# Kernel tuning notes

Measured on AMD Instinct MI355X. Metric: run time of the kernel, lower is better.

Reference implementation:

```python
import jax, jax.numpy as jnp
import numpy as np

B, T, IN, H = 262144, 15, 1, 64
BN_EPS = 1e-5


def _lstm_layer(xs, w_ih, w_hh, b):
    """xs: [T, B, in] -> (hs [T, B, H], h_last [B, H]). torch gate order i,f,g,o."""
    Bn = xs.shape[1]
    h0 = jnp.zeros((Bn, H), xs.dtype)
    c0 = jnp.zeros((Bn, H), xs.dtype)

    def step(carry, x_t):
        h, c = carry
        z = x_t @ w_ih.T + h @ w_hh.T + b  # [B, 4H]
        i, f, g, o = jnp.split(z, 4, axis=-1)
        i = jax.nn.sigmoid(i)
        f = jax.nn.sigmoid(f)
        g = jnp.tanh(g)
        o = jax.nn.sigmoid(o)
        c = f * c + i * g
        h = o * jnp.tanh(c)
        return (h, c), h

    (h_last, _), hs = jax.lax.scan(step, (h0, c0), xs)
    return hs, h_last


def setup_inputs() -> dict:
    key = jax.random.key(0)
    ks = jax.random.split(key, 12)
    s = 0.1  # weight init scale ~ 1/sqrt(H)
    return {
        "x": jax.random.normal(ks[0], (B, T, IN), jnp.float32),
        "bn_gamma": jnp.ones((T,), jnp.float32),
        "bn_beta": jnp.zeros((T,), jnp.float32),
        "w_ih0": jax.random.normal(ks[1], (4 * H, IN), jnp.float32) * s,
        "w_hh0": jax.random.normal(ks[2], (4 * H, H), jnp.float32) * s,
        "b_ih0": jax.random.normal(ks[3], (4 * H,), jnp.float32) * s,
        "b_hh0": jax.random.normal(ks[4], (4 * H,), jnp.float32) * s,
        "w_ih1": jax.random.normal(ks[5], (4 * H, H), jnp.float32) * s,
        "w_hh1": jax.random.normal(ks[6], (4 * H, H), jnp.float32) * s,
        "b_ih1": jax.random.normal(ks[7], (4 * H,), jnp.float32) * s,
        "b_hh1": jax.random.normal(ks[8], (4 * H,), jnp.float32) * s,
        "fc_w": jax.random.normal(ks[9], (H, H), jnp.float32) * s,
        "fc_b": jax.random.normal(ks[10], (H,), jnp.float32) * s,
    }


def reference(x, bn_gamma, bn_beta, w_ih0, w_hh0, b_ih0, b_hh0,
              w_ih1, w_hh1, b_ih1, b_hh1, fc_w, fc_b):
    # BatchNorm1d(num_steps) on [B, T, IN]: channels = T, stats over (B, IN) (training mode, biased var)
    mean = jnp.mean(x, axis=(0, 2), keepdims=True)
    var = jnp.var(x, axis=(0, 2), keepdims=True)
    xh = (x - mean) * jax.lax.rsqrt(var + BN_EPS)
    xh = xh * bn_gamma[None, :, None] + bn_beta[None, :, None]

    xs = jnp.transpose(xh, (1, 0, 2))  # [T, B, IN] (time-major for scan)
    hs1, _ = _lstm_layer(xs, w_ih0, w_hh0, b_ih0 + b_hh0)
    _, h_last = _lstm_layer(hs1, w_ih1, w_hh1, b_ih1 + b_hh1)

    # fc1 on last timestep + exact (erf) GELU, matching torch F.gelu default
    y = h_last @ fc_w.T + fc_b
    return jax.nn.gelu(y, approximate=False)
```

## Files before the change

kernel.cpp:

```cpp
#include <hip/hip_runtime.h>
#include <math.h>


typedef __attribute__((ext_vector_type(8))) short short8;
typedef __attribute__((ext_vector_type(4))) float f32x4;

namespace {
constexpr int kB = 262144;
constexpr int kT = 15;
constexpr int kTiles = kB / 32;
constexpr int kGrid = 512;
constexpr int WS_SS = 0;
constexpr int WS_B0 = 32;
constexpr int WS_B1 = 288;
constexpr int WS_FCT = 1024;
constexpr int WS_STATS = 5200;
constexpr int WS_BF = 8192;
}

#if __has_builtin(__builtin_amdgcn_exp2f)
__device__ __forceinline__ float exp2x(float x) {
  return __builtin_amdgcn_exp2f(x);
}
#else
__device__ __forceinline__ float exp2x(float x) {
  float r;
  asm("v_exp_f32 %0, %1\n\ts_nop 1" : "=v"(r) : "v"(x));
  return r;
}
#endif

__device__ __forceinline__ ushort f2bf(float f) {
  unsigned u = __float_as_uint(f);
  unsigned r = (u + 0x7fffu + ((u >> 16) & 1u)) >> 16;
  return (ushort)r;
}
__device__ __forceinline__ ushort f2bf_fast(float f) {
  unsigned r;
  asm("v_cvt_pk_bf16_f32 %0, %1, %2" : "=v"(r) : "v"(f), "v"(f));
  return (ushort)r;
}
__device__ __forceinline__ float gscale(int g) {
  return (g == 2) ? 2.88539008177792681472f : -1.44269504088896340736f;
}

__global__ void prep_kernel(const float* __restrict__ w_hh0,
                            const float* __restrict__ w_ih1,
                            const float* __restrict__ w_hh1,
                            const float* __restrict__ b_ih0,
                            const float* __restrict__ b_hh0,
                            const float* __restrict__ b_ih1,
                            const float* __restrict__ b_hh1,
                            const float* __restrict__ fc_w,
                            float* __restrict__ ws) {
  const int stride = gridDim.x * blockDim.x;
  const int t0 = blockIdx.x * blockDim.x + threadIdx.x;
  ushort* bf = (ushort*)(ws + WS_BF);
  for (int i = t0; i < 96 * 512; i += stride) {
    int chunk = i >> 9, lane = (i >> 3) & 63, j = i & 7;
    float v;
    int n;
    if (chunk < 32) {
      int ks = chunk >> 4, nt = chunk & 15;
      int k = 32 * ks + 8 * (lane >> 4) + j;
      n = 16 * nt + (lane & 15);
      v = w_hh0[n * 64 + k];
    } else {
      int c2 = chunk - 32;
      int ks = c2 >> 4, nt = c2 & 15;
      int k = 32 * ks + 8 * (lane >> 4) + j;
      n = 16 * nt + (lane & 15);
      v = (k < 64) ? w_ih1[n * 64 + k] : w_hh1[n * 64 + (k - 64)];
    }
    bf[i] = f2bf(v * gscale(n >> 6));
  }
  for (int i = t0; i < 4096; i += stride) {
    int u = i >> 6, o = i & 63;
    ws[WS_FCT + i] = fc_w[o * 64 + u];
  }
  for (int i = t0; i < 256; i += stride) {
    float sc = gscale(i >> 6);
    ws[WS_B0 + i] = (b_ih0[i] + b_hh0[i]) * sc;
    ws[WS_B1 + i] = (b_ih1[i] + b_hh1[i]) * sc;
  }
  for (int i = t0; i < 32; i += stride) ws[WS_STATS + i] = 0.f;
}

__global__ void bn_sums_kernel(const float* __restrict__ x,
                               float* __restrict__ ws) {
  __shared__ float ls[16], lq[16];
  const int tid = threadIdx.x;
  if (tid < 16) { ls[tid] = 0.f; lq[tid] = 0.f; }
  __syncthreads();
  const float4* x4 = (const float4*)x;
  const int c0 = (blockIdx.x * 256 + tid) * 15;
  float s[15], q[15];
#pragma unroll
  for (int t = 0; t < 15; ++t) { s[t] = 0.f; q[t] = 0.f; }
#pragma unroll
  for (int c = 0; c < 15; ++c) {
    float4 v = x4[c0 + c];
    s[(4 * c + 0) % 15] += v.x; q[(4 * c + 0) % 15] += v.x * v.x;
    s[(4 * c + 1) % 15] += v.y; q[(4 * c + 1) % 15] += v.y * v.y;
    s[(4 * c + 2) % 15] += v.z; q[(4 * c + 2) % 15] += v.z * v.z;
    s[(4 * c + 3) % 15] += v.w; q[(4 * c + 3) % 15] += v.w * v.w;
  }
#pragma unroll
  for (int t = 0; t < 15; ++t) {
    atomicAdd(&ls[t], s[t]);
    atomicAdd(&lq[t], q[t]);
  }
  __syncthreads();
  if (tid < 15) {
    atomicAdd(&ws[WS_STATS + tid], ls[tid]);
    atomicAdd(&ws[WS_STATS + 16 + tid], lq[tid]);
  }
}

__global__ void bn_final_kernel(const float* __restrict__ gamma,
                                const float* __restrict__ beta,
                                float* __restrict__ ws) {
  int t = threadIdx.x;
  if (t < 15) {
    const float inv = 1.f / (float)kB;
    float mean = ws[WS_STATS + t] * inv;
    float var = ws[WS_STATS + 16 + t] * inv - mean * mean;
    float sc = gamma[t] * rsqrtf(var + 1e-5f);
    ws[WS_SS + t] = sc;
    ws[WS_SS + 16 + t] = beta[t] - mean * sc;
  }
}

__global__ __launch_bounds__(256, 2) void lstm_fused_kernel(
    const float* __restrict__ x, const float* __restrict__ w_ih0,
    const float* __restrict__ fc_b, const float* __restrict__ ws,
    float* __restrict__ out) {
  __shared__ ushort h0b[2][32 * 64];
  __shared__ ushort h1b[2][32 * 64];
  __shared__ float xsf[32 * 17];
  __shared__ float h1f[32 * 68];

  const int tid = threadIdx.x;
  const int lane = tid & 63;
  const int wv = tid >> 6;
  const int grp = lane >> 4;
  const int l15 = lane & 15;
  const int u = wv * 16 + l15;

  float b0g[4], b1g[4], w0g[4];
#pragma unroll
  for (int j = 0; j < 4; ++j) {
    b0g[j] = ws[WS_B0 + u + 64 * j];
    b1g[j] = ws[WS_B1 + u + 64 * j];
    w0g[j] = w_ih0[u + 64 * j] * gscale(j);
  }
  const short8* bfr = (const short8*)(ws + WS_BF);
  short8 bL0[8], bL1[16];
#pragma unroll
  for (int ks = 0; ks < 2; ++ks)
#pragma unroll
    for (int j = 0; j < 4; ++j)
      bL0[ks * 4 + j] = bfr[(ks * 16 + wv + 4 * j) * 64 + lane];
#pragma unroll
  for (int ks = 0; ks < 4; ++ks)
#pragma unroll
    for (int j = 0; j < 4; ++j)
      bL1[ks * 4 + j] = bfr[(32 + ks * 16 + wv + 4 * j) * 64 + lane];

  auto ldA = [&](const ushort* buf, int mt, int kbase) -> short8 {
    int row = l15 + 16 * mt;
    int off = (kbase + 8 * grp) ^ ((row & 7) << 3);
    return *(const short8*)&buf[row * 64 + off];
  };

#pragma unroll 1
  for (int tile = blockIdx.x; tile < kTiles; tile += kGrid) {
    const int bm0 = tile * 32;

    for (int i = tid; i < 32 * kT; i += 256) {
      float v = x[(size_t)bm0 * kT + i];
      int m = i / 15, tt = i - m * 15;
      xsf[m * 17 + tt] = v * ws[WS_SS + tt] + ws[WS_SS + 16 + tt];
    }
    for (int i = tid; i < 1024; i += 256) {
      ((unsigned*)h0b[1])[i] = 0u;
      ((unsigned*)h1b[1])[i] = 0u;
    }

    float c0r[8], c1r[8];
#pragma unroll
    for (int i = 0; i < 8; ++i) { c0r[i] = 0.f; c1r[i] = 0.f; }

    __syncthreads();

#pragma unroll 1
    for (int t = 0; t < kT; ++t) {
      const int p = t & 1;
      const ushort* h0rd = h0b[p ^ 1];
      ushort* h0wr = h0b[p];
      const ushort* h1rd = h1b[p ^ 1];
      ushort* h1wr = h1b[p];

      f32x4 acc[2][4];
#pragma unroll
      for (int mt = 0; mt < 2; ++mt)
#pragma unroll
        for (int r = 0; r < 4; ++r) {
          float xv = xsf[(16 * mt + 4 * grp + r) * 17 + t];
#pragma unroll
          for (int j = 0; j < 4; ++j) acc[mt][j][r] = fmaf(xv, w0g[j], b0g[j]);
        }
#pragma unroll
      for (int ks = 0; ks < 2; ++ks) {
        short8 a0 = ldA(h0rd, 0, 32 * ks);
        short8 a1 = ldA(h0rd, 1, 32 * ks);
#pragma unroll
        for (int j = 0; j < 4; ++j) {
          acc[0][j] = __builtin_amdgcn_mfma_f32_16x16x32_bf16(a0, bL0[ks * 4 + j], acc[0][j], 0, 0, 0);
          acc[1][j] = __builtin_amdgcn_mfma_f32_16x16x32_bf16(a1, bL0[ks * 4 + j], acc[1][j], 0, 0, 0);
        }
      }
#pragma unroll
      for (int mt = 0; mt < 2; ++mt)
#pragma unroll
        for (int r = 0; r < 4; ++r) {
          int row = 16 * mt + 4 * grp + r;
          float ig = __builtin_amdgcn_rcpf(1.f + exp2x(acc[mt][0][r]));
          float fg = __builtin_amdgcn_rcpf(1.f + exp2x(acc[mt][1][r]));
          float gg = 1.f - 2.f * __builtin_amdgcn_rcpf(1.f + exp2x(acc[mt][2][r]));
          float og = __builtin_amdgcn_rcpf(1.f + exp2x(acc[mt][3][r]));
          float c = fmaf(fg, c0r[mt * 4 + r], ig * gg);
          c0r[mt * 4 + r] = c;
          float th = 1.f - 2.f * __builtin_amdgcn_rcpf(1.f + exp2x(c * 2.88539008177792681472f));
          h0wr[row * 64 + (u ^ ((row & 7) << 3))] = f2bf_fast(og * th);
        }
      __syncthreads();

#pragma unroll
      for (int mt = 0; mt < 2; ++mt)
#pragma unroll
        for (int j = 0; j < 4; ++j)
#pragma unroll
          for (int r = 0; r < 4; ++r) acc[mt][j][r] = b1g[j];
#pragma unroll
      for (int ks = 0; ks < 2; ++ks) {
        short8 a0 = ldA(h0wr, 0, 32 * ks);
        short8 a1 = ldA(h0wr, 1, 32 * ks);
#pragma unroll
        for (int j = 0; j < 4; ++j) {
          acc[0][j] = __builtin_amdgcn_mfma_f32_16x16x32_bf16(a0, bL1[ks * 4 + j], acc[0][j], 0, 0, 0);
          acc[1][j] = __builtin_amdgcn_mfma_f32_16x16x32_bf16(a1, bL1[ks * 4 + j], acc[1][j], 0, 0, 0);
        }
      }
#pragma unroll
      for (int ks = 2; ks < 4; ++ks) {
        short8 a0 = ldA(h1rd, 0, 32 * (ks - 2));
        short8 a1 = ldA(h1rd, 1, 32 * (ks - 2));
#pragma unroll
        for (int j = 0; j < 4; ++j) {
          acc[0][j] = __builtin_amdgcn_mfma_f32_16x16x32_bf16(a0, bL1[ks * 4 + j], acc[0][j], 0, 0, 0);
          acc[1][j] = __builtin_amdgcn_mfma_f32_16x16x32_bf16(a1, bL1[ks * 4 + j], acc[1][j], 0, 0, 0);
        }
      }
#pragma unroll
      for (int mt = 0; mt < 2; ++mt)
#pragma unroll
        for (int r = 0; r < 4; ++r) {
          int row = 16 * mt + 4 * grp + r;
          float ig = __builtin_amdgcn_rcpf(1.f + exp2x(acc[mt][0][r]));
          float fg = __builtin_amdgcn_rcpf(1.f + exp2x(acc[mt][1][r]));
          float gg = 1.f - 2.f * __builtin_amdgcn_rcpf(1.f + exp2x(acc[mt][2][r]));
          float og = __builtin_amdgcn_rcpf(1.f + exp2x(acc[mt][3][r]));
          float c = fmaf(fg, c1r[mt * 4 + r], ig * gg);
          c1r[mt * 4 + r] = c;
          float th = 1.f - 2.f * __builtin_amdgcn_rcpf(1.f + exp2x(c * 2.88539008177792681472f));
          float h = og * th;
          if (t < kT - 1) {
            h1wr[row * 64 + (u ^ ((row & 7) << 3))] = f2bf_fast(h);
          } else {
            h1f[row * 68 + u] = h;
          }
        }
    }
    __syncthreads();

    {
      const int o = tid & 63;
      const int ms = tid >> 6;
      float yv[8];
      float fb = fc_b[o];
#pragma unroll
      for (int i = 0; i < 8; ++i) yv[i] = fb;
#pragma unroll 1
      for (int u0 = 0; u0 < 64; u0 += 4) {
        float q0 = ws[WS_FCT + (u0 + 0) * 64 + o];
        float q1 = ws[WS_FCT + (u0 + 1) * 64 + o];
        float q2 = ws[WS_FCT + (u0 + 2) * 64 + o];
        float q3 = ws[WS_FCT + (u0 + 3) * 64 + o];
#pragma unroll
        for (int i = 0; i < 8; ++i) {
          const float4 hq = *(const float4*)&h1f[(ms * 8 + i) * 68 + u0];
          yv[i] = fmaf(hq.x, q0, yv[i]);
          yv[i] = fmaf(hq.y, q1, yv[i]);
          yv[i] = fmaf(hq.z, q2, yv[i]);
          yv[i] = fmaf(hq.w, q3, yv[i]);
        }
      }
#pragma unroll
      for (int i = 0; i < 8; ++i) {
        float v = yv[i];
        float g = 0.5f * v * (1.f + erff(v * 0.70710678118654752f));
        out[(size_t)(bm0 + ms * 8 + i) * 64 + o] = g;
      }
    }
  }
}

extern "C" void kernel_launch(void* const* d_in, const int* in_sizes, int n_in,
                              void* d_out, int out_size, void* d_ws, size_t ws_size,
                              hipStream_t stream) {
  const float* x = (const float*)d_in[0];
  const float* bn_gamma = (const float*)d_in[1];
  const float* bn_beta = (const float*)d_in[2];
  const float* w_ih0 = (const float*)d_in[3];
  const float* w_hh0 = (const float*)d_in[4];
  const float* b_ih0 = (const float*)d_in[5];
  const float* b_hh0 = (const float*)d_in[6];
  const float* w_ih1 = (const float*)d_in[7];
  const float* w_hh1 = (const float*)d_in[8];
  const float* b_ih1 = (const float*)d_in[9];
  const float* b_hh1 = (const float*)d_in[10];
  const float* fc_w = (const float*)d_in[11];
  const float* fc_b = (const float*)d_in[12];
  float* ws = (float*)d_ws;
  float* out = (float*)d_out;

  hipLaunchKernelGGL(prep_kernel, dim3(64), dim3(256), 0, stream,
                     w_hh0, w_ih1, w_hh1, b_ih0, b_hh0, b_ih1, b_hh1, fc_w, ws);
  hipLaunchKernelGGL(bn_sums_kernel, dim3(256), dim3(256), 0, stream, x, ws);
  hipLaunchKernelGGL(bn_final_kernel, dim3(1), dim3(64), 0, stream,
                     bn_gamma, bn_beta, ws);
  hipLaunchKernelGGL(lstm_fused_kernel, dim3(kGrid), dim3(256), 0, stream,
                     x, w_ih0, fc_b, ws, out);
}
```

Before: 813.8 us.

## Software-pipeline LSTM layers so layer-0 step t+1 overlaps layer-1 step t

The time loop is restructured so that each iteration runs layer 1 at step t and also issues the layer-0 MFMAs and gate math for step t+1. A prologue computes layer-0 step 0. This removes one of the two block barriers per timestep and gives the scheduler independent MFMA and transcendental work to interleave. In exchange it holds two sets of accumulators live at once, which raises register pressure and could reduce occupancy.

```diff
diff --git a/kernel.cpp b/kernel.cpp
--- a/kernel.cpp
+++ b/kernel.cpp
@@ -173,6 +173,46 @@
     return *(const short8*)&buf[row * 64 + off];
   };
 
+  f32x4 accL0[2][4], accL1[2][4];
+
+  auto doL0 = [&](int tt, const ushort* h0src) {
+#pragma unroll
+    for (int mt = 0; mt < 2; ++mt)
+#pragma unroll
+      for (int r = 0; r < 4; ++r) {
+        float xv = xsf[(16 * mt + 4 * grp + r) * 17 + tt];
+#pragma unroll
+        for (int j = 0; j < 4; ++j) accL0[mt][j][r] = fmaf(xv, w0g[j], b0g[j]);
+      }
+#pragma unroll
+    for (int ks = 0; ks < 2; ++ks) {
+      short8 a0 = ldA(h0src, 0, 32 * ks);
+      short8 a1 = ldA(h0src, 1, 32 * ks);
+#pragma unroll
+      for (int j = 0; j < 4; ++j) {
+        accL0[0][j] = __builtin_amdgcn_mfma_f32_16x16x32_bf16(a0, bL0[ks * 4 + j], accL0[0][j], 0, 0, 0);
+        accL0[1][j] = __builtin_amdgcn_mfma_f32_16x16x32_bf16(a1, bL0[ks * 4 + j], accL0[1][j], 0, 0, 0);
+      }
+    }
+  };
+
+  auto doGates = [&](f32x4 (&acc)[2][4], float* cr, ushort* dst) {
+#pragma unroll
+    for (int mt = 0; mt < 2; ++mt)
+#pragma unroll
+      for (int r = 0; r < 4; ++r) {
+        int row = 16 * mt + 4 * grp + r;
+        float ig = __builtin_amdgcn_rcpf(1.f + exp2x(acc[mt][0][r]));
+        float fg = __builtin_amdgcn_rcpf(1.f + exp2x(acc[mt][1][r]));
+        float gg = 1.f - 2.f * __builtin_amdgcn_rcpf(1.f + exp2x(acc[mt][2][r]));
+        float og = __builtin_amdgcn_rcpf(1.f + exp2x(acc[mt][3][r]));
+        float c = fmaf(fg, cr[mt * 4 + r], ig * gg);
+        cr[mt * 4 + r] = c;
+        float th = 1.f - 2.f * __builtin_amdgcn_rcpf(1.f + exp2x(c * 2.88539008177792681472f));
+        dst[row * 64 + (u ^ ((row & 7) << 3))] = f2bf_fast(og * th);
+      }
+  };
+
 #pragma unroll 1
   for (int tile = blockIdx.x; tile < kTiles; tile += kGrid) {
     const int bm0 = tile * 32;
@@ -193,94 +233,66 @@
 
     __syncthreads();
 
+    doL0(0, h0b[1]);
+    doGates(accL0, c0r, h0b[0]);
+    __syncthreads();
+
 #pragma unroll 1
     for (int t = 0; t < kT; ++t) {
       const int p = t & 1;
-      const ushort* h0rd = h0b[p ^ 1];
-      ushort* h0wr = h0b[p];
-      const ushort* h1rd = h1b[p ^ 1];
-      ushort* h1wr = h1b[p];
-
-      f32x4 acc[2][4];
+
 #pragma unroll
       for (int mt = 0; mt < 2; ++mt)
 #pragma unroll
-        for (int r = 0; r < 4; ++r) {
-          float xv = xsf[(16 * mt + 4 * grp + r) * 17 + t];
-#pragma unroll
-          for (int j = 0; j < 4; ++j) acc[mt][j][r] = fmaf(xv, w0g[j], b0g[j]);
+        for (int j = 0; j < 4; ++j)
+#pragma unroll
+          for (int r = 0; r < 4; ++r) accL1[mt][j][r] = b1g[j];
+#pragma unroll
+      for (int ks = 0; ks < 2; ++ks) {
+        short8 a0 = ldA(h0b[p], 0, 32 * ks);
+        short8 a1 = ldA(h0b[p], 1, 32 * ks);
+#pragma unroll
+        for (int j = 0; j < 4; ++j) {
+          accL1[0][j] = __builtin_amdgcn_mfma_f32_16x16x32_bf16(a0, bL1[ks * 4 + j], accL1[0][j], 0, 0, 0);
+          accL1[1][j] = __builtin_amdgcn_mfma_f32_16x16x32_bf16(a1, bL1[ks * 4 + j], accL1[1][j], 0, 0, 0);
         }
-#pragma unroll
-      for (int ks = 0; ks < 2; ++ks) {
-        short8 a0 = ldA(h0rd, 0, 32 * ks);
-        short8 a1 = ldA(h0rd, 1, 32 * ks);
+      }
+#pragma unroll
+      for (int ks = 2; ks < 4; ++ks) {
+        short8 a0 = ldA(h1b[p ^ 1], 0, 32 * (ks - 2));
+        short8 a1 = ldA(h1b[p ^ 1], 1, 32 * (ks - 2));
 #pragma unroll
         for (int j = 0; j < 4; ++j) {
-          acc[0][j] = __builtin_amdgcn_mfma_f32_16x16x32_bf16(a0, bL0[ks * 4 + j], acc[0][j], 0, 0, 0);
-          acc[1][j] = __builtin_amdgcn_mfma_f32_16x16x32_bf16(a1, bL0[ks * 4 + j], acc[1][j], 0, 0, 0);
+          accL1[0][j] = __builtin_amdgcn_mfma_f32_16x16x32_bf16(a0, bL1[ks * 4 + j], accL1[0][j], 0, 0, 0);
+          accL1[1][j] = __builtin_amdgcn_mfma_f32_16x16x32_bf16(a1, bL1[ks * 4 + j], accL1[1][j], 0, 0, 0);
         }
       }
-#pragma unroll
-      for (int mt = 0; mt < 2; ++mt)
-#pragma unroll
-        for (int r = 0; r < 4; ++r) {
-          int row = 16 * mt + 4 * grp + r;
-          float ig = __builtin_amdgcn_rcpf(1.f + exp2x(acc[mt][0][r]));
-          float fg = __builtin_amdgcn_rcpf(1.f + exp2x(acc[mt][1][r]));
-          float gg = 1.f - 2.f * __builtin_amdgcn_rcpf(1.f + exp2x(acc[mt][2][r]));
-          float og = __builtin_amdgcn_rcpf(1.f + exp2x(acc[mt][3][r]));
-          float c = fmaf(fg, c0r[mt * 4 + r], ig * gg);
-          c0r[mt * 4 + r] = c;
-          float th = 1.f - 2.f * __builtin_amdgcn_rcpf(1.f + exp2x(c * 2.88539008177792681472f));
-          h0wr[row * 64 + (u ^ ((row & 7) << 3))] = f2bf_fast(og * th);
-        }
-      __syncthreads();
-
-#pragma unroll
-      for (int mt = 0; mt < 2; ++mt)
-#pragma unroll
-        for (int j = 0; j < 4; ++j)
-#pragma unroll
-          for (int r = 0; r < 4; ++r) acc[mt][j][r] = b1g[j];
-#pragma unroll
-      for (int ks = 0; ks < 2; ++ks) {
-        short8 a0 = ldA(h0wr, 0, 32 * ks);
-        short8 a1 = ldA(h0wr, 1, 32 * ks);
-#pragma unroll
-        for (int j = 0; j < 4; ++j) {
-          acc[0][j] = __builtin_amdgcn_mfma_f32_16x16x32_bf16(a0, bL1[ks * 4 + j], acc[0][j], 0, 0, 0);
-          acc[1][j] = __builtin_amdgcn_mfma_f32_16x16x32_bf16(a1, bL1[ks * 4 + j], acc[1][j], 0, 0, 0);
-        }
-      }
-#pragma unroll
-      for (int ks = 2; ks < 4; ++ks) {
-        short8 a0 = ldA(h1rd, 0, 32 * (ks - 2));
-        short8 a1 = ldA(h1rd, 1, 32 * (ks - 2));
-#pragma unroll
-        for (int j = 0; j < 4; ++j) {
-          acc[0][j] = __builtin_amdgcn_mfma_f32_16x16x32_bf16(a0, bL1[ks * 4 + j], acc[0][j], 0, 0, 0);
-          acc[1][j] = __builtin_amdgcn_mfma_f32_16x16x32_bf16(a1, bL1[ks * 4 + j], acc[1][j], 0, 0, 0);
-        }
-      }
-#pragma unroll
-      for (int mt = 0; mt < 2; ++mt)
-#pragma unroll
-        for (int r = 0; r < 4; ++r) {
-          int row = 16 * mt + 4 * grp + r;
-          float ig = __builtin_amdgcn_rcpf(1.f + exp2x(acc[mt][0][r]));
-          float fg = __builtin_amdgcn_rcpf(1.f + exp2x(acc[mt][1][r]));
-          float gg = 1.f - 2.f * __builtin_amdgcn_rcpf(1.f + exp2x(acc[mt][2][r]));
-          float og = __builtin_amdgcn_rcpf(1.f + exp2x(acc[mt][3][r]));
-          float c = fmaf(fg, c1r[mt * 4 + r], ig * gg);
-          c1r[mt * 4 + r] = c;
-          float th = 1.f - 2.f * __builtin_amdgcn_rcpf(1.f + exp2x(c * 2.88539008177792681472f));
-          float h = og * th;
-          if (t < kT - 1) {
-            h1wr[row * 64 + (u ^ ((row & 7) << 3))] = f2bf_fast(h);
-          } else {
-            h1f[row * 68 + u] = h;
+
+      if (t < kT - 1) doL0(t + 1, h0b[p]);
+
+      if (t < kT - 1) {
+        doGates(accL1, c1r, h1b[p]);
+      } else {
+#pragma unroll
+        for (int mt = 0; mt < 2; ++mt)
+#pragma unroll
+          for (int r = 0; r < 4; ++r) {
+            int row = 16 * mt + 4 * grp + r;
+            float ig = __builtin_amdgcn_rcpf(1.f + exp2x(accL1[mt][0][r]));
+            float fg = __builtin_amdgcn_rcpf(1.f + exp2x(accL1[mt][1][r]));
+            float gg = 1.f - 2.f * __builtin_amdgcn_rcpf(1.f + exp2x(accL1[mt][2][r]));
+            float og = __builtin_amdgcn_rcpf(1.f + exp2x(accL1[mt][3][r]));
+            float c = fmaf(fg, c1r[mt * 4 + r], ig * gg);
+            c1r[mt * 4 + r] = c;
+            float th = 1.f - 2.f * __builtin_amdgcn_rcpf(1.f + exp2x(c * 2.88539008177792681472f));
+            h1f[row * 68 + u] = og * th;
           }
-        }
+      }
+
+      if (t < kT - 1) {
+        doGates(accL0, c0r, h0b[p ^ 1]);
+        __syncthreads();
+      }
     }
     __syncthreads();
 
```

New measurement: 1.184 ms. 1.45x slower.
